# Kernel tuning notes

Hardware: AMD Instinct MI355X
Metric: run time of the kernel (lower is better)

## Reference

```python
import jax, jax.numpy as jnp
import numpy as np

B, N, E = 4, 10000, 170000
F_IN, F, H = 256, 128, 4
LEAKY_SLOPE = 0.2  # TF default alpha for tf.nn.leaky_relu


def setup_inputs() -> dict:
    key = jax.random.key(0)
    ks = jax.random.split(key, 6)
    x = jax.random.normal(ks[0], (B, N, F_IN), jnp.float32)
    src = jnp.sort(jax.random.randint(ks[1], (E,), 0, N, jnp.int32))
    dst = jax.random.randint(ks[2], (E,), 0, N, jnp.int32)
    W_mlp = jax.random.normal(ks[3], (H, F_IN, F), jnp.float32) / np.float32(np.sqrt(F_IN))
    b_mlp = jnp.zeros((H, F), jnp.float32)
    W_attn = jax.random.normal(ks[4], (H, 2 * F, 1), jnp.float32) / np.float32(np.sqrt(2 * F))
    return {"x": x, "W_mlp": W_mlp, "b_mlp": b_mlp, "W_attn": W_attn, "src": src, "dst": dst}


def reference(x, W_mlp, b_mlp, W_attn, src, dst):
    n_edges = src.shape[0]
    batch = x.shape[0]
    # per-head node transform: [B,H,N,F]
    h = jnp.einsum('bnf,hfe->bhne', x, W_mlp) + b_mlp[None, :, None, :]
    # split attention kernel: score = leaky_relu([h_src||h_dst] @ W_attn)
    a_src = W_attn[:, :F, 0]  # [H,F]
    a_dst = W_attn[:, F:, 0]  # [H,F]
    # faithful quirk: the original normalizes and scatters attention from the
    # LAST batch element only (attention_scores[-1]) and applies it to all batches
    hl = h[-1]  # [H,N,F]
    p_src = jnp.einsum('hnf,hf->hn', hl, a_src)
    p_dst = jnp.einsum('hnf,hf->hn', hl, a_dst)
    s = p_src[:, src] + p_dst[:, dst]                 # [H,E]
    e = jnp.exp(jnp.clip(jax.nn.leaky_relu(s, LEAKY_SLOPE), -2.0, 2.0))
    denom = jax.ops.segment_sum(e.T, src, num_segments=N).T  # [H,N]
    norm = e / denom[:, src]                          # [H,E]
    outs = []
    for hi in range(H):  # small fixed head loop (limits peak memory)
        g = jnp.take(h[:, hi], dst, axis=1) * norm[hi][None, :, None]  # [B,E,F]
        g = jnp.swapaxes(g, 0, 1).reshape(n_edges, batch * F)          # [E,B*F]
        agg = jax.ops.segment_sum(g, src, num_segments=N)              # [N,B*F]
        outs.append(agg.reshape(N, batch, F).transpose(1, 0, 2))       # [B,N,F]
    return jnp.concatenate(outs, axis=-1)  # [B,N,H*F]
```

## Files before the change

### kernel.cpp

```cpp
#include <hip/hip_runtime.h>
#include <hip/hip_bf16.h>

constexpr int Bq  = 4;
constexpr int Nn  = 10000;
constexpr int Eq  = 170000;
constexpr int FIN = 256;
constexpr int Ff  = 128;
constexpr int Hh  = 4;
constexpr int Mrows = Nn * Bq;
constexpr int C   = Hh * Ff;
constexpr float LEAKY = 0.2f;

typedef short short4v __attribute__((ext_vector_type(4)));
typedef short short8  __attribute__((ext_vector_type(8)));
typedef float f32x4   __attribute__((ext_vector_type(4)));

static __device__ __forceinline__ unsigned short f2bf(float f) {
    unsigned int u = __float_as_uint(f);
    u = u + 0x7fffu + ((u >> 16) & 1u);
    return (unsigned short)(u >> 16);
}
static __device__ __forceinline__ float bf2f(unsigned short b) {
    return __uint_as_float(((unsigned int)b) << 16);
}

__global__ __launch_bounds__(256) void prep_kernel(
    const float* __restrict__ W, const float* __restrict__ Wattn,
    const float* __restrict__ bmlp, const int* __restrict__ src,
    unsigned short* __restrict__ Wf, float* __restrict__ wa,
    float* __restrict__ bsd, int* __restrict__ row_start)
{
    int bid = blockIdx.x, t = threadIdx.x;
    if (bid < 512) {
        int cc = bid;
        int k = t;
        float v = W[(size_t)(cc >> 7) * FIN * Ff + (size_t)k * Ff + (cc & 127)];
        int w = cc >> 7, j = (cc >> 4) & 7, ln = cc & 15;
        int ks = k >> 5, quad = (k >> 3) & 3, el = k & 7;
        size_t u = ((size_t)((w * 8 + j) * 8 + ks) * 4 + quad) * 16 + ln;
        Wf[u * 8 + el] = f2bf(v);
    } else if (bid == 512) {
        int hi = t >> 6, kb = t & 63;
        #pragma unroll
        for (int i = 0; i < 4; ++i) {
            int k = kb + i * 64;
            float ss = 0.f, sd = 0.f;
            const float* wrow = W + ((size_t)hi * FIN + k) * Ff;
            const float* as = Wattn + hi * 2 * Ff;
            const float* ad = as + Ff;
            for (int f = 0; f < Ff; f += 4) {
                float4 wv = *(const float4*)(wrow + f);
                float4 av = *(const float4*)(as + f);
                float4 dv = *(const float4*)(ad + f);
                ss += wv.x * av.x + wv.y * av.y + wv.z * av.z + wv.w * av.w;
                sd += wv.x * dv.x + wv.y * dv.y + wv.z * dv.z + wv.w * dv.w;
            }
            wa[(0 * 4 + hi) * FIN + k] = ss;
            wa[(1 * 4 + hi) * FIN + k] = sd;
        }
        if (t < 8) {
            int v = t & 1, hh = t >> 1;
            float s = 0.f;
            for (int f = 0; f < Ff; ++f)
                s += bmlp[hh * Ff + f] * Wattn[hh * 2 * Ff + v * Ff + f];
            bsd[v * 4 + hh] = s;
        }
    } else {
        int n = (bid - 513) * 256 + t;
        if (n > Nn) return;
        int lo = 0, hi = Eq;
        while (lo < hi) { int mid = (lo + hi) >> 1; if (src[mid] < n) lo = mid + 1; else hi = mid; }
        row_start[n] = lo;
    }
}

__global__ __launch_bounds__(256) void xprep_proj_kernel(
    const float* __restrict__ X, const float* __restrict__ wa,
    const float* __restrict__ bsd, unsigned short* __restrict__ Xb,
    float* __restrict__ psT, float* __restrict__ pdT)
{
    int n0 = blockIdx.x * 8;
    int t  = threadIdx.x;
    int r  = t >> 5;
    int c  = t & 31;
    int k8 = c * 8;
    float s[8];
    #pragma unroll
    for (int i = 0; i < 8; ++i) s[i] = 0.f;

    #pragma unroll
    for (int b = 0; b < Bq; ++b) {
        const float* p = X + ((size_t)b * Nn + n0 + r) * FIN + k8;
        float4 v0 = *(const float4*)p, v1 = *(const float4*)(p + 4);
        short8 v;
        v[0] = (short)f2bf(v0.x); v[1] = (short)f2bf(v0.y);
        v[2] = (short)f2bf(v0.z); v[3] = (short)f2bf(v0.w);
        v[4] = (short)f2bf(v1.x); v[5] = (short)f2bf(v1.y);
        v[6] = (short)f2bf(v1.z); v[7] = (short)f2bf(v1.w);
        *(short8*)(Xb + ((size_t)(n0 + r) * Bq + b) * FIN + k8) = v;
        if (b == Bq - 1) {
            #pragma unroll
            for (int i = 0; i < 8; ++i) {
                const float* w = wa + (size_t)i * FIN + k8;
                float4 w0 = *(const float4*)w, w1 = *(const float4*)(w + 4);
                s[i] = v0.x * w0.x + v0.y * w0.y + v0.z * w0.z + v0.w * w0.w
                     + v1.x * w1.x + v1.y * w1.y + v1.z * w1.z + v1.w * w1.w;
            }
        }
    }
    #pragma unroll
    for (int off = 1; off < 32; off <<= 1)
        #pragma unroll
        for (int i = 0; i < 8; ++i) s[i] += __shfl_xor(s[i], off, 64);
    if (c == 0) {
        int n = n0 + r;
        #pragma unroll
        for (int hi = 0; hi < 4; ++hi) {
            psT[n * 4 + hi] = s[hi]     + bsd[hi];
            pdT[n * 4 + hi] = s[4 + hi] + bsd[4 + hi];
        }
    }
}

__global__ __launch_bounds__(256) void edge_denom_kernel(
    const int* __restrict__ dst, const int* __restrict__ row_start,
    const float* __restrict__ psT, const float* __restrict__ pdT,
    float* __restrict__ eed, float* __restrict__ denom)
{
    int wv = threadIdx.x >> 6, t = threadIdx.x & 63;
    int n = blockIdx.x * 4 + wv;
    int e0 = row_start[n], e1 = row_start[n + 1];
    float4 ps = *(const float4*)(psT + (size_t)n * 4);
    float4 acc = {0.f, 0.f, 0.f, 0.f};
    for (int e = e0 + t; e < e1; e += 64) {
        int d = dst[e];
        float4 pd = *(const float4*)(pdT + (size_t)d * 4);
        float4 ev;
        { float sc = ps.x + pd.x; float lr = sc > 0.f ? sc : LEAKY * sc;
          ev.x = __expf(fminf(fmaxf(lr, -2.f), 2.f)); }
        { float sc = ps.y + pd.y; float lr = sc > 0.f ? sc : LEAKY * sc;
          ev.y = __expf(fminf(fmaxf(lr, -2.f), 2.f)); }
        { float sc = ps.z + pd.z; float lr = sc > 0.f ? sc : LEAKY * sc;
          ev.z = __expf(fminf(fmaxf(lr, -2.f), 2.f)); }
        { float sc = ps.w + pd.w; float lr = sc > 0.f ? sc : LEAKY * sc;
          ev.w = __expf(fminf(fmaxf(lr, -2.f), 2.f)); }
        *(float4*)(eed + (size_t)e * 4) = ev;
        acc.x += ev.x; acc.y += ev.y; acc.z += ev.z; acc.w += ev.w;
    }
    #pragma unroll
    for (int off = 1; off < 64; off <<= 1) {
        acc.x += __shfl_xor(acc.x, off, 64);
        acc.y += __shfl_xor(acc.y, off, 64);
        acc.z += __shfl_xor(acc.z, off, 64);
        acc.w += __shfl_xor(acc.w, off, 64);
    }
    if (t == 0) *(float4*)(denom + (size_t)n * 4) = acc;
    float4 inv;
    inv.x = acc.x != 0.f ? 1.f / acc.x : 0.f;
    inv.y = acc.y != 0.f ? 1.f / acc.y : 0.f;
    inv.z = acc.z != 0.f ? 1.f / acc.z : 0.f;
    inv.w = acc.w != 0.f ? 1.f / acc.w : 0.f;
    for (int e = e0 + t; e < e1; e += 64) {
        float4 ev = *(const float4*)(eed + (size_t)e * 4);
        ev.x *= inv.x; ev.y *= inv.y; ev.z *= inv.z; ev.w *= inv.w;
        *(float4*)(eed + (size_t)e * 4) = ev;
    }
}

__global__ __launch_bounds__(256) void gather_kernel(
    const unsigned short* __restrict__ Xb, const float* __restrict__ eed,
    const int* __restrict__ row_start, const int* __restrict__ dst,
    unsigned short* __restrict__ Gx)
{
    int n = blockIdx.x, t = threadIdx.x;
    int e0 = row_start[n], e1 = row_start[n + 1];

    float acc[4][4];
    #pragma unroll
    for (int hi = 0; hi < 4; ++hi)
        #pragma unroll
        for (int j = 0; j < 4; ++j) acc[hi][j] = 0.f;

    const float4* eed4 = (const float4*)eed;
    int off = t * 4;

    int e = e0;
    for (; e + 4 <= e1; e += 4) {
        int d0 = dst[e], d1 = dst[e + 1], d2 = dst[e + 2], d3 = dst[e + 3];
        short4v v0 = *(const short4v*)(Xb + (size_t)d0 * 1024 + off);
        short4v v1 = *(const short4v*)(Xb + (size_t)d1 * 1024 + off);
        short4v v2 = *(const short4v*)(Xb + (size_t)d2 * 1024 + off);
        short4v v3 = *(const short4v*)(Xb + (size_t)d3 * 1024 + off);
        float4 ev0 = eed4[e], ev1 = eed4[e + 1], ev2 = eed4[e + 2], ev3 = eed4[e + 3];
        float w[4][4] = {
            {ev0.x, ev0.y, ev0.z, ev0.w},
            {ev1.x, ev1.y, ev1.z, ev1.w},
            {ev2.x, ev2.y, ev2.z, ev2.w},
            {ev3.x, ev3.y, ev3.z, ev3.w}};
        #pragma unroll
        for (int j = 0; j < 4; ++j) {
            float f0 = bf2f((unsigned short)v0[j]);
            float f1 = bf2f((unsigned short)v1[j]);
            float f2 = bf2f((unsigned short)v2[j]);
            float f3 = bf2f((unsigned short)v3[j]);
            #pragma unroll
            for (int hi = 0; hi < 4; ++hi)
                acc[hi][j] += f0 * w[0][hi] + f1 * w[1][hi] + f2 * w[2][hi] + f3 * w[3][hi];
        }
    }
    for (; e < e1; ++e) {
        int d0 = dst[e];
        short4v v0 = *(const short4v*)(Xb + (size_t)d0 * 1024 + off);
        float4 ev0 = eed4[e];
        #pragma unroll
        for (int j = 0; j < 4; ++j) {
            float f = bf2f((unsigned short)v0[j]);
            acc[0][j] += f * ev0.x; acc[1][j] += f * ev0.y;
            acc[2][j] += f * ev0.z; acc[3][j] += f * ev0.w;
        }
    }

    int b = t >> 6, k0 = (t & 63) * 4;
    #pragma unroll
    for (int hi = 0; hi < 4; ++hi) {
        short4v o;
        #pragma unroll
        for (int j = 0; j < 4; ++j) o[j] = (short)f2bf(acc[hi][j]);
        *(short4v*)(Gx + ((size_t)hi * Mrows + (size_t)n * 4 + b) * FIN + k0) = o;
    }
}

__global__ __launch_bounds__(256) void gemm2_kernel(
    const unsigned short* __restrict__ Gx, const unsigned short* __restrict__ Wf,
    const float* __restrict__ bias, const float* __restrict__ denom,
    float* __restrict__ out)
{
    __shared__ unsigned short As[64][264];

    const int hi = blockIdx.y;
    const int r0 = blockIdx.x * 64;
    const int tid = threadIdx.x;
    const int wave = tid >> 6, lane = tid & 63;
    const int quad = lane >> 4, ln = lane & 15;

    const unsigned short* Arows = Gx + ((size_t)hi * Mrows + r0) * FIN;
    #pragma unroll
    for (int i = 0; i < 8; ++i) {
        int u = tid + i * 256;
        int row = u >> 5, cu = u & 31;
        *(short8*)&As[row][cu * 8] = *(const short8*)(Arows + (size_t)row * FIN + cu * 8);
    }
    __syncthreads();

    f32x4 macc[8];
    #pragma unroll
    for (int j = 0; j < 8; ++j) macc[j] = (f32x4){0.f, 0.f, 0.f, 0.f};

    const short8* Wf8 = (const short8*)Wf;
    const int m0 = wave * 16;
    #pragma unroll
    for (int ks = 0; ks < 8; ++ks) {
        short8 a = *(const short8*)&As[m0 + ln][ks * 32 + quad * 8];
        #pragma unroll
        for (int j = 0; j < 8; ++j) {
            short8 bf = Wf8[(size_t)((hi * 8 + j) * 8 + ks) * 64 + lane];
            macc[j] = __builtin_amdgcn_mfma_f32_16x16x32_bf16(a, bf, macc[j], 0, 0, 0);
        }
    }

    #pragma unroll
    for (int j = 0; j < 8; ++j) {
        int colf = j * 16 + ln;
        float bv = bias[hi * Ff + colf];
        #pragma unroll
        for (int r = 0; r < 4; ++r) {
            int m = m0 + quad * 4 + r;
            int g = r0 + m;
            int nn = g >> 2, bb = g & 3;
            float flag = denom[(size_t)nn * 4 + hi] != 0.f ? 1.f : 0.f;
            out[((size_t)bb * Nn + nn) * C + hi * Ff + colf] = macc[j][r] + bv * flag;
        }
    }
}

extern "C" void kernel_launch(void* const* d_in, const int* in_sizes, int n_in,
                              void* d_out, int out_size, void* d_ws, size_t ws_size,
                              hipStream_t stream)
{
    const float* x      = (const float*)d_in[0];
    const float* W_mlp  = (const float*)d_in[1];
    const float* b_mlp  = (const float*)d_in[2];
    const float* W_attn = (const float*)d_in[3];
    const int*   src    = (const int*)d_in[4];
    const int*   dst    = (const int*)d_in[5];
    float* out = (float*)d_out;

    unsigned short* Xb  = (unsigned short*)d_ws;
    unsigned short* Wf  = Xb + (size_t)Nn * Bq * FIN;
    unsigned short* Gx  = Wf + (size_t)C * FIN;
    float* eed   = (float*)(Gx + (size_t)Hh * Mrows * FIN);
    float* psT   = eed + (size_t)Eq * 4;
    float* pdT   = psT + (size_t)Nn * 4;
    float* denom = pdT + (size_t)Nn * 4;
    float* wa    = denom + (size_t)Nn * 4;
    float* bsd   = wa + 2 * 4 * FIN;
    int*   row_st = (int*)(bsd + 16);

    hipLaunchKernelGGL(prep_kernel, dim3(553), dim3(256), 0, stream,
                       W_mlp, W_attn, b_mlp, src, Wf, wa, bsd, row_st);
    hipLaunchKernelGGL(xprep_proj_kernel, dim3(Nn / 8), dim3(256), 0, stream,
                       x, wa, bsd, Xb, psT, pdT);
    hipLaunchKernelGGL(edge_denom_kernel, dim3(Nn / 4), dim3(256), 0, stream,
                       dst, row_st, psT, pdT, eed, denom);
    hipLaunchKernelGGL(gather_kernel, dim3(Nn), dim3(256), 0, stream,
                       Xb, eed, row_st, dst, Gx);
    hipLaunchKernelGGL(gemm2_kernel, dim3(Mrows / 64, Hh), dim3(256), 0, stream,
                       Gx, Wf, b_mlp, denom, out);
}
```

Baseline: 231.2 us.

## Store bf16 X batch-major, gather per wave per batch, stage GEMM output

The bf16 copy of X is now kept in the original batch-major layout [B,N,FIN] rather than node-interleaved. The gather kernel maps one wave to one node and launches a separate grid slice per batch, so each wave reads 512-byte rows from a single batch plane; the aim is better L2 locality per batch. The GEMM epilogue writes results to LDS first and then emits coalesced float4 rows to the output instead of scattered scalar stores. In exchange, edge indices and weights are reloaded once per batch, and the epilogue adds an extra LDS round trip and barriers.

```diff
diff --git a/kernel.cpp b/kernel.cpp
--- a/kernel.cpp
+++ b/kernel.cpp
@@ -90,14 +90,15 @@
 
     #pragma unroll
     for (int b = 0; b < Bq; ++b) {
-        const float* p = X + ((size_t)b * Nn + n0 + r) * FIN + k8;
+        size_t lin = ((size_t)b * Nn + n0 + r) * FIN + k8;
+        const float* p = X + lin;
         float4 v0 = *(const float4*)p, v1 = *(const float4*)(p + 4);
         short8 v;
         v[0] = (short)f2bf(v0.x); v[1] = (short)f2bf(v0.y);
         v[2] = (short)f2bf(v0.z); v[3] = (short)f2bf(v0.w);
         v[4] = (short)f2bf(v1.x); v[5] = (short)f2bf(v1.y);
         v[6] = (short)f2bf(v1.z); v[7] = (short)f2bf(v1.w);
-        *(short8*)(Xb + ((size_t)(n0 + r) * Bq + b) * FIN + k8) = v;
+        *(short8*)(Xb + lin) = v;
         if (b == Bq - 1) {
             #pragma unroll
             for (int i = 0; i < 8; ++i) {
@@ -172,8 +173,12 @@
     const int* __restrict__ row_start, const int* __restrict__ dst,
     unsigned short* __restrict__ Gx)
 {
-    int n = blockIdx.x, t = threadIdx.x;
+    int wv = threadIdx.x >> 6, t = threadIdx.x & 63;
+    int n = blockIdx.x * 4 + wv;
+    int b = blockIdx.y;
     int e0 = row_start[n], e1 = row_start[n + 1];
+    const unsigned short* Xbb = Xb + (size_t)b * Nn * FIN;
+    int off = t * 4;
 
     float acc[4][4];
     #pragma unroll
@@ -182,35 +187,29 @@
         for (int j = 0; j < 4; ++j) acc[hi][j] = 0.f;
 
     const float4* eed4 = (const float4*)eed;
-    int off = t * 4;
-
     int e = e0;
     for (; e + 4 <= e1; e += 4) {
         int d0 = dst[e], d1 = dst[e + 1], d2 = dst[e + 2], d3 = dst[e + 3];
-        short4v v0 = *(const short4v*)(Xb + (size_t)d0 * 1024 + off);
-        short4v v1 = *(const short4v*)(Xb + (size_t)d1 * 1024 + off);
-        short4v v2 = *(const short4v*)(Xb + (size_t)d2 * 1024 + off);
-        short4v v3 = *(const short4v*)(Xb + (size_t)d3 * 1024 + off);
+        short4v v0 = *(const short4v*)(Xbb + (size_t)d0 * FIN + off);
+        short4v v1 = *(const short4v*)(Xbb + (size_t)d1 * FIN + off);
+        short4v v2 = *(const short4v*)(Xbb + (size_t)d2 * FIN + off);
+        short4v v3 = *(const short4v*)(Xbb + (size_t)d3 * FIN + off);
         float4 ev0 = eed4[e], ev1 = eed4[e + 1], ev2 = eed4[e + 2], ev3 = eed4[e + 3];
-        float w[4][4] = {
-            {ev0.x, ev0.y, ev0.z, ev0.w},
-            {ev1.x, ev1.y, ev1.z, ev1.w},
-            {ev2.x, ev2.y, ev2.z, ev2.w},
-            {ev3.x, ev3.y, ev3.z, ev3.w}};
         #pragma unroll
         for (int j = 0; j < 4; ++j) {
             float f0 = bf2f((unsigned short)v0[j]);
             float f1 = bf2f((unsigned short)v1[j]);
             float f2 = bf2f((unsigned short)v2[j]);
             float f3 = bf2f((unsigned short)v3[j]);
-            #pragma unroll
-            for (int hi = 0; hi < 4; ++hi)
-                acc[hi][j] += f0 * w[0][hi] + f1 * w[1][hi] + f2 * w[2][hi] + f3 * w[3][hi];
+            acc[0][j] += f0 * ev0.x + f1 * ev1.x + f2 * ev2.x + f3 * ev3.x;
+            acc[1][j] += f0 * ev0.y + f1 * ev1.y + f2 * ev2.y + f3 * ev3.y;
+            acc[2][j] += f0 * ev0.z + f1 * ev1.z + f2 * ev2.z + f3 * ev3.z;
+            acc[3][j] += f0 * ev0.w + f1 * ev1.w + f2 * ev2.w + f3 * ev3.w;
         }
     }
     for (; e < e1; ++e) {
         int d0 = dst[e];
-        short4v v0 = *(const short4v*)(Xb + (size_t)d0 * 1024 + off);
+        short4v v0 = *(const short4v*)(Xbb + (size_t)d0 * FIN + off);
         float4 ev0 = eed4[e];
         #pragma unroll
         for (int j = 0; j < 4; ++j) {
@@ -220,13 +219,12 @@
         }
     }
 
-    int b = t >> 6, k0 = (t & 63) * 4;
     #pragma unroll
     for (int hi = 0; hi < 4; ++hi) {
         short4v o;
         #pragma unroll
         for (int j = 0; j < 4; ++j) o[j] = (short)f2bf(acc[hi][j]);
-        *(short4v*)(Gx + ((size_t)hi * Mrows + (size_t)n * 4 + b) * FIN + k0) = o;
+        *(short4v*)(Gx + ((size_t)hi * Mrows + (size_t)n * 4 + b) * FIN + off) = o;
     }
 }
 
@@ -267,7 +265,9 @@
             macc[j] = __builtin_amdgcn_mfma_f32_16x16x32_bf16(a, bf, macc[j], 0, 0, 0);
         }
     }
-
+    __syncthreads();
+
+    float* Lf = (float*)As;
     #pragma unroll
     for (int j = 0; j < 8; ++j) {
         int colf = j * 16 + ln;
@@ -275,11 +275,21 @@
         #pragma unroll
         for (int r = 0; r < 4; ++r) {
             int m = m0 + quad * 4 + r;
-            int g = r0 + m;
-            int nn = g >> 2, bb = g & 3;
+            int nn = (r0 + m) >> 2;
             float flag = denom[(size_t)nn * 4 + hi] != 0.f ? 1.f : 0.f;
-            out[((size_t)bb * Nn + nn) * C + hi * Ff + colf] = macc[j][r] + bv * flag;
-        }
+            Lf[m * 132 + colf] = macc[j][r] + bv * flag;
+        }
+    }
+    __syncthreads();
+
+    #pragma unroll
+    for (int i = 0; i < 8; ++i) {
+        int u = tid + i * 256;
+        int row = u >> 5, cu = u & 31;
+        int g = r0 + row;
+        int nn = g >> 2, bb = g & 3;
+        float4 v = *(const float4*)&Lf[row * 132 + cu * 4];
+        *(float4*)(out + ((size_t)bb * Nn + nn) * C + hi * Ff + cu * 4) = v;
     }
 }
 
@@ -296,7 +306,7 @@
     float* out = (float*)d_out;
 
     unsigned short* Xb  = (unsigned short*)d_ws;
-    unsigned short* Wf  = Xb + (size_t)Nn * Bq * FIN;
+    unsigned short* Wf  = Xb + (size_t)Bq * Nn * FIN;
     unsigned short* Gx  = Wf + (size_t)C * FIN;
     float* eed   = (float*)(Gx + (size_t)Hh * Mrows * FIN);
     float* psT   = eed + (size_t)Eq * 4;
@@ -312,7 +322,7 @@
                        x, wa, bsd, Xb, psT, pdT);
     hipLaunchKernelGGL(edge_denom_kernel, dim3(Nn / 4), dim3(256), 0, stream,
                        dst, row_st, psT, pdT, eed, denom);
-    hipLaunchKernelGGL(gather_kernel, dim3(Nn), dim3(256), 0, stream,
+    hipLaunchKernelGGL(gather_kernel, dim3(Nn / 4, Bq), dim3(256), 0, stream,
                        Xb, eed, row_st, dst, Gx);
     hipLaunchKernelGGL(gemm2_kernel, dim3(Mrows / 64, Hh), dim3(256), 0, stream,
                        Gx, Wf, b_mlp, denom, out);
```

Measured after the change: 235.7 us. About the same (+2.0%).
